# Kernel optimization log

Measured on AMD Instinct MI355X. Metric: run time of the kernel, lower is better.

Reference implementation:

```python
import jax, jax.numpy as jnp
import numpy as np

D_MODEL = 2048
SEQ_LEN = 16   # R is built for context_window=16 in the original module
BATCH = 256


def make_rotary_matrix(m, d):
    # Faithful to get_rotary_matrix: theta = 10000 ** (-2*(i-1)/d)  (note the i-1 bug kept)
    pos = np.arange(m, dtype=np.float64)[:, None]            # [m,1]
    i = np.arange(d // 2, dtype=np.float64)[None, :]         # [1,d/2]
    theta = 10000.0 ** (-2.0 * (i - 1.0) / d)
    ang = pos * theta                                         # [m, d/2]
    cos, sin = np.cos(ang), np.sin(ang)
    R = np.zeros((m, d, d), dtype=np.float32)
    idx = np.arange(d // 2)
    R[:, 2 * idx, 2 * idx] = cos
    R[:, 2 * idx, 2 * idx + 1] = -sin
    R[:, 2 * idx + 1, 2 * idx] = sin
    R[:, 2 * idx + 1, 2 * idx + 1] = cos
    return jnp.asarray(R)


def setup_inputs() -> dict:
    key = jax.random.key(0)
    kx, kq, kk, kv = jax.random.split(key, 4)
    s = 1.0 / np.sqrt(D_MODEL)
    return {
        "x": jax.random.normal(kx, (BATCH, SEQ_LEN, D_MODEL), dtype=jnp.float32),
        "w_q": jax.random.normal(kq, (D_MODEL, D_MODEL), dtype=jnp.float32) * s,
        "w_k": jax.random.normal(kk, (D_MODEL, D_MODEL), dtype=jnp.float32) * s,
        "w_v": jax.random.normal(kv, (D_MODEL, D_MODEL), dtype=jnp.float32) * s,
    }


def reference(x, w_q, w_k, w_v):
    b, m, d = x.shape
    R = make_rotary_matrix(SEQ_LEN, d)[:m]                    # [m,d,d]
    # nn.Linear(bias=False): y = x @ W^T
    q = jnp.einsum("bmd,ed->bme", x, w_q)
    k = jnp.einsum("bmd,ed->bme", x, w_k)
    v = jnp.einsum("bmd,ed->bme", x, w_v)
    # dense per-position rotary rotation via bmm: (q.transpose(0,1) @ R[:m]).transpose(0,1)
    q_rot = jnp.einsum("bmd,mde->bme", q, R)
    k_rot = jnp.einsum("bmd,mde->bme", k, R)
    # scaled_dot_product_attention (dropout treated as eval-mode / disabled)
    scores = jnp.einsum("bme,bne->bmn", q_rot, k_rot) / jnp.sqrt(jnp.float32(d))
    attn = jax.nn.softmax(scores, axis=-1)
    return jnp.einsum("bmn,bne->bme", attn, v)
```

## Files before the change

### kernel.cpp

```cpp
#include <hip/hip_runtime.h>


#define D 2048
#define SEQLEN 16
#define NBATCH 256
#define NROWS (NBATCH * SEQLEN)
#define NX (NROWS * D)
#define NW (D * D)

#define BM 128
#define BN 192
#define BK 64
#define NKT (D / BK)
#define LDSPB ((BM + BN) * BK)

typedef __attribute__((ext_vector_type(8))) short bf16x8;
typedef __attribute__((ext_vector_type(4))) float f32x4;

__device__ __forceinline__ unsigned short f32_to_bf16(float f) {
  unsigned u = __float_as_uint(f);
  unsigned r = 0x7fffu + ((u >> 16) & 1u);
  return (unsigned short)((u + r) >> 16);
}
__device__ __forceinline__ float bf16lo_to_f32(unsigned u) { return __uint_as_float(u << 16); }
__device__ __forceinline__ float bf16hi_to_f32(unsigned u) { return __uint_as_float(u & 0xffff0000u); }

__device__ __forceinline__ bool detect_f32(const ushort* __restrict__ w) {
  int crazy = 0;
#pragma unroll
  for (int i = 0; i < 64; ++i) {
    float v = __uint_as_float((unsigned)w[i] << 16);
    if (!(__builtin_fabsf(v) < 256.0f)) ++crazy;
  }
  return crazy >= 3;
}

__device__ __forceinline__ void glds16(const void* g, void* l) {
  __builtin_amdgcn_global_load_lds(
      (const __attribute__((address_space(1))) void*)g,
      (__attribute__((address_space(3))) void*)l, 16, 0, 0);
}

__global__ __launch_bounds__(256) void convert_inputs(
    const void* __restrict__ x, const void* __restrict__ wq,
    const void* __restrict__ wk, const void* __restrict__ wv,
    ushort* __restrict__ xb, ushort* __restrict__ wqb,
    ushort* __restrict__ wkb, ushort* __restrict__ wvb) {
  if (!detect_f32((const ushort*)wq)) return;
  const float* srcs[4] = {(const float*)x, (const float*)wq, (const float*)wk, (const float*)wv};
  ushort* dsts[4] = {xb, wqb, wkb, wvb};
  const int ns[4] = {NX, NW, NW, NW};
  const int stride = gridDim.x * blockDim.x;
#pragma unroll
  for (int s = 0; s < 4; ++s) {
    const float* __restrict__ src = srcs[s];
    ushort* __restrict__ dst = dsts[s];
    const int n8 = ns[s] / 8;
    for (int i = blockIdx.x * blockDim.x + threadIdx.x; i < n8; i += stride) {
      float4 a = ((const float4*)src)[i * 2];
      float4 b = ((const float4*)src)[i * 2 + 1];
      uint4 o;
      o.x = (unsigned)f32_to_bf16(a.x) | ((unsigned)f32_to_bf16(a.y) << 16);
      o.y = (unsigned)f32_to_bf16(a.z) | ((unsigned)f32_to_bf16(a.w) << 16);
      o.z = (unsigned)f32_to_bf16(b.x) | ((unsigned)f32_to_bf16(b.y) << 16);
      o.w = (unsigned)f32_to_bf16(b.z) | ((unsigned)f32_to_bf16(b.w) << 16);
      ((uint4*)dst)[i] = o;
    }
  }
}

__global__ __launch_bounds__(256, 2) void qkv_rope_gemm(
    const void* __restrict__ Xr, const void* __restrict__ Wqr,
    const void* __restrict__ Wkr, const void* __restrict__ Wvr,
    const ushort* __restrict__ xb, const ushort* __restrict__ wqb,
    const ushort* __restrict__ wkb, const ushort* __restrict__ wvb,
    ushort* __restrict__ Ov, float* __restrict__ Sp) {
  __shared__ __align__(16) ushort lds[2][LDSPB];

  const bool f32in = detect_f32((const ushort*)Wqr);
  const ushort* __restrict__ X  = f32in ? xb  : (const ushort*)Xr;
  const ushort* __restrict__ Wq = f32in ? wqb : (const ushort*)Wqr;
  const ushort* __restrict__ Wk = f32in ? wkb : (const ushort*)Wkr;
  const ushort* __restrict__ Wv = f32in ? wvb : (const ushort*)Wvr;

  const int m0 = (blockIdx.x >> 5) * BM;
  const int eb = blockIdx.x & 31;
  const int e0 = eb * 64;

  const int t = threadIdx.x;
  const int wave = t >> 6, lane = t & 63;
  const int quad = lane >> 4, l16 = lane & 15;
  const int wr = wave >> 1, wc = wave & 1;

  const int srow = t >> 3;
  const int scol = ((t & 7) ^ (srow & 7)) * 8;
  const ushort* gA = X + (size_t)(m0 + srow) * D + scol;
  const ushort* gB[6];
#pragma unroll
  for (int c = 0; c < 6; ++c) {
    const ushort* Wz = (c < 2) ? Wq : (c < 4) ? Wk : Wv;
    gB[c] = Wz + (size_t)(e0 + (c & 1) * 32 + srow) * D + scol;
  }

  f32x4 acc[4][6] = {};

  auto STAGE = [&](int b, int kt) {
    const int kc = kt * BK;
#pragma unroll
    for (int c = 0; c < 4; ++c)
      glds16(gA + (size_t)c * 32 * D + kc, &lds[b][c * 2048 + t * 8]);
#pragma unroll
    for (int c = 0; c < 6; ++c)
      glds16(gB[c] + kc, &lds[b][BM * BK + c * 2048 + t * 8]);
  };

  STAGE(0, 0);
  STAGE(1, 1);

  const int swz = (l16 & 7) << 3;

  for (int kt = 0; kt < NKT; ++kt) {
    const int cur = kt & 1;

    if (kt < NKT - 1) asm volatile("s_waitcnt vmcnt(10)" ::: "memory");
    else              asm volatile("s_waitcnt vmcnt(0)"  ::: "memory");
    __builtin_amdgcn_s_barrier();
    __builtin_amdgcn_sched_barrier(0);

    const ushort* Ab = &lds[cur][0];
    const ushort* Bb = &lds[cur][BM * BK];

    bf16x8 af2[2][4], bfr2[2][6];
#pragma unroll
    for (int ks = 0; ks < 2; ++ks) {
      const int ko = (ks * 32 + quad * 8) ^ swz;
#pragma unroll
      for (int f = 0; f < 4; ++f)
        af2[ks][f] = *(const bf16x8*)(Ab + (wr * 64 + f * 16 + l16) * 64 + ko);
#pragma unroll
      for (int g = 0; g < 6; ++g)
        bfr2[ks][g] = *(const bf16x8*)(Bb + (wc * 96 + g * 16 + l16) * 64 + ko);
    }
    asm volatile("s_waitcnt lgkmcnt(0)" ::: "memory");
    __builtin_amdgcn_s_barrier();
    if (kt + 2 < NKT) STAGE(cur, kt + 2);
    __builtin_amdgcn_sched_barrier(0);

    __builtin_amdgcn_s_setprio(1);
#pragma unroll
    for (int ks = 0; ks < 2; ++ks)
#pragma unroll
      for (int f = 0; f < 4; ++f)
#pragma unroll
        for (int g = 0; g < 6; ++g)
          acc[f][g] = __builtin_amdgcn_mfma_f32_16x16x32_bf16(
              af2[ks][f], bfr2[ks][g], acc[f][g], 0, 0, 0);
    __builtin_amdgcn_s_setprio(0);
  }

  ushort* qk_lds = &lds[0][0];
#pragma unroll
  for (int g = 0; g < 6; ++g) {
    const int ncol = wc * 96 + g * 16;
    const int z = ncol >> 6;
    const int el = (ncol & 63) + l16;
    const int eg = e0 + el;
    if (z < 2) {
      const float theta = exp2f(-0.012976281620653759f * ((float)(eg >> 1) - 1.0f));
      float cs[4], sn[4];
#pragma unroll
      for (int r = 0; r < 4; ++r)
        __sincosf((float)(quad * 4 + r) * theta, &sn[r], &cs[r]);
#pragma unroll
      for (int f = 0; f < 4; ++f) {
#pragma unroll
        for (int r = 0; r < 4; ++r) {
          float v = acc[f][g][r];
          float p = __shfl_xor(v, 1);
          float o = (eg & 1) ? (v * cs[r] - p * sn[r])
                             : (v * cs[r] + p * sn[r]);
          const int row = wr * 64 + f * 16 + quad * 4 + r;
          const int colw = el ^ ((row & 7) << 3);
          qk_lds[z * 8192 + row * 64 + colw] = f32_to_bf16(o);
        }
      }
    } else {
#pragma unroll
      for (int f = 0; f < 4; ++f) {
        const size_t rbase = (size_t)(m0 + wr * 64 + f * 16 + quad * 4) * D;
#pragma unroll
        for (int r = 0; r < 4; ++r)
          Ov[rbase + (size_t)r * D + eg] = f32_to_bf16(acc[f][g][r]);
      }
    }
  }
  __syncthreads();

  const int gb0 = (m0 >> 4);
#pragma unroll
  for (int bb = 0; bb < 2; ++bb) {
    const int bi = wave * 2 + bb;
    const int row = bi * 16 + l16;
    f32x4 s = {0.f, 0.f, 0.f, 0.f};
#pragma unroll
    for (int ks = 0; ks < 2; ++ks) {
      const int ko = (ks * 32 + quad * 8) ^ swz;
      bf16x8 aq = *(const bf16x8*)(qk_lds + row * 64 + ko);
      bf16x8 bk = *(const bf16x8*)(qk_lds + 8192 + row * 64 + ko);
      s = __builtin_amdgcn_mfma_f32_16x16x32_bf16(aq, bk, s, 0, 0, 0);
    }
    float* sp = Sp + ((size_t)(eb * NBATCH + gb0 + bi) << 8);
#pragma unroll
    for (int r = 0; r < 4; ++r)
      sp[(quad * 4 + r) * 16 + l16] = s[r];
  }
}

__global__ __launch_bounds__(256) void rope_attention(
    const float* __restrict__ Sp, const ushort* __restrict__ V,
    const void* __restrict__ Wqr, void* __restrict__ OutRaw) {
  __shared__ float at[16][16];
  const bool f32out = detect_f32((const ushort*)Wqr);
  const int b = blockIdx.x;
  const int t = threadIdx.x;

  {
    const int m = t >> 4, n = t & 15;
    float s = 0.f;
#pragma unroll
    for (int ebi = 0; ebi < 32; ++ebi)
      s += Sp[((size_t)(ebi * NBATCH + b) << 8) + t];
    s *= 0.02209708691207961f;
    float mx = s;
#pragma unroll
    for (int off = 8; off; off >>= 1) mx = fmaxf(mx, __shfl_xor(mx, off, 16));
    float e = __expf(s - mx);
    float sum = e;
#pragma unroll
    for (int off = 8; off; off >>= 1) sum += __shfl_xor(sum, off, 16);
    at[m][n] = e / sum;
  }
  __syncthreads();

  const ushort* Vb = V + (size_t)b * (SEQLEN * D);
  const int e0 = t * 8;
  uint4 vr[16];
#pragma unroll
  for (int n = 0; n < 16; ++n)
    vr[n] = *(const uint4*)(Vb + n * D + e0);

  for (int m = 0; m < 16; ++m) {
    float av[8] = {0.f, 0.f, 0.f, 0.f, 0.f, 0.f, 0.f, 0.f};
#pragma unroll
    for (int n = 0; n < 16; ++n) {
      const float a = at[m][n];
      const uint4 u = vr[n];
      av[0] = fmaf(a, bf16lo_to_f32(u.x), av[0]);
      av[1] = fmaf(a, bf16hi_to_f32(u.x), av[1]);
      av[2] = fmaf(a, bf16lo_to_f32(u.y), av[2]);
      av[3] = fmaf(a, bf16hi_to_f32(u.y), av[3]);
      av[4] = fmaf(a, bf16lo_to_f32(u.z), av[4]);
      av[5] = fmaf(a, bf16hi_to_f32(u.z), av[5]);
      av[6] = fmaf(a, bf16lo_to_f32(u.w), av[6]);
      av[7] = fmaf(a, bf16hi_to_f32(u.w), av[7]);
    }
    if (f32out) {
      float* Ob = (float*)OutRaw + (size_t)b * (SEQLEN * D) + m * D + e0;
      float4 o0 = {av[0], av[1], av[2], av[3]};
      float4 o1 = {av[4], av[5], av[6], av[7]};
      ((float4*)Ob)[0] = o0;
      ((float4*)Ob)[1] = o1;
    } else {
      uint4 o;
      o.x = (unsigned)f32_to_bf16(av[0]) | ((unsigned)f32_to_bf16(av[1]) << 16);
      o.y = (unsigned)f32_to_bf16(av[2]) | ((unsigned)f32_to_bf16(av[3]) << 16);
      o.z = (unsigned)f32_to_bf16(av[4]) | ((unsigned)f32_to_bf16(av[5]) << 16);
      o.w = (unsigned)f32_to_bf16(av[6]) | ((unsigned)f32_to_bf16(av[7]) << 16);
      *(uint4*)((ushort*)OutRaw + (size_t)b * (SEQLEN * D) + m * D + e0) = o;
    }
  }
}

extern "C" void kernel_launch(void* const* d_in, const int* in_sizes, int n_in,
                              void* d_out, int out_size, void* d_ws, size_t ws_size,
                              hipStream_t stream) {
  const void* x  = d_in[0];
  const void* wq = d_in[1];
  const void* wk = d_in[2];
  const void* wv = d_in[3];
  ushort* ws = (ushort*)d_ws;
  ushort* xb  = ws;
  ushort* wqb = ws + NX;
  ushort* wkb = ws + NX + NW;
  ushort* wvb = ws + NX + 2 * (size_t)NW;
  ushort* v   = ws + NX + 3 * (size_t)NW;
  float*  Sp  = (float*)(ws + 2 * (size_t)NX + 3 * (size_t)NW);

  convert_inputs<<<1536, 256, 0, stream>>>(x, wq, wk, wv, xb, wqb, wkb, wvb);
  qkv_rope_gemm<<<dim3(1024), 256, 0, stream>>>(x, wq, wk, wv, xb, wqb, wkb, wvb, v, Sp);
  rope_attention<<<NBATCH, 256, 0, stream>>>(Sp, v, wq, (ushort*)d_out);
}
```

Baseline: 228.9 us.

## Enlarge QKV GEMM tile to 256 rows with 512 threads and split MFMA phases

The fused QKV+RoPE GEMM block grows from 128x192 to 256x192 using 8 waves. Each block now loads one 64-row slice of each of Wq, Wk and Wv, and covers twice as many X rows, so weight tiles are shared across more rows and fewer blocks reload them. The inner loop is also restructured: B fragments are loaded once, A fragments are loaded in two halves, and each half is followed by its MFMAs between barriers, so LDS reads interleave with compute. The cost is a larger LDS footprint, about 115KB per block. That likely allows only one block per CU despite the launch bound of two, and the added barriers per k-step may cost synchronisation time.

```diff
diff --git a/kernel.cpp b/kernel.cpp
--- a/kernel.cpp
+++ b/kernel.cpp
@@ -8,7 +8,7 @@
 #define NX (NROWS * D)
 #define NW (D * D)
 
-#define BM 128
+#define BM 256
 #define BN 192
 #define BK 64
 #define NKT (D / BK)
@@ -69,13 +69,13 @@
   }
 }
 
-__global__ __launch_bounds__(256, 2) void qkv_rope_gemm(
+__global__ __launch_bounds__(512, 2) void qkv_rope_gemm(
     const void* __restrict__ Xr, const void* __restrict__ Wqr,
     const void* __restrict__ Wkr, const void* __restrict__ Wvr,
     const ushort* __restrict__ xb, const ushort* __restrict__ wqb,
     const ushort* __restrict__ wkb, const ushort* __restrict__ wvb,
     ushort* __restrict__ Ov, float* __restrict__ Sp) {
-  __shared__ __align__(16) ushort lds[2][LDSPB];
+  __shared__ __align__(16) ushort ldsraw[2 * LDSPB];
 
   const bool f32in = detect_f32((const ushort*)Wqr);
   const ushort* __restrict__ X  = f32in ? xb  : (const ushort*)Xr;
@@ -90,28 +90,27 @@
   const int t = threadIdx.x;
   const int wave = t >> 6, lane = t & 63;
   const int quad = lane >> 4, l16 = lane & 15;
-  const int wr = wave >> 1, wc = wave & 1;
+  const int wr = wave >> 2, wc = wave & 3;
 
   const int srow = t >> 3;
   const int scol = ((t & 7) ^ (srow & 7)) * 8;
   const ushort* gA = X + (size_t)(m0 + srow) * D + scol;
-  const ushort* gB[6];
-#pragma unroll
-  for (int c = 0; c < 6; ++c) {
-    const ushort* Wz = (c < 2) ? Wq : (c < 4) ? Wk : Wv;
-    gB[c] = Wz + (size_t)(e0 + (c & 1) * 32 + srow) * D + scol;
-  }
-
-  f32x4 acc[4][6] = {};
+  const ushort* gB[3];
+  gB[0] = Wq + (size_t)(e0 + srow) * D + scol;
+  gB[1] = Wk + (size_t)(e0 + srow) * D + scol;
+  gB[2] = Wv + (size_t)(e0 + srow) * D + scol;
+
+  f32x4 acc[8][3] = {};
 
   auto STAGE = [&](int b, int kt) {
+    ushort* base = ldsraw + b * LDSPB;
     const int kc = kt * BK;
 #pragma unroll
     for (int c = 0; c < 4; ++c)
-      glds16(gA + (size_t)c * 32 * D + kc, &lds[b][c * 2048 + t * 8]);
-#pragma unroll
-    for (int c = 0; c < 6; ++c)
-      glds16(gB[c] + kc, &lds[b][BM * BK + c * 2048 + t * 8]);
+      glds16(gA + (size_t)c * 64 * D + kc, base + c * 4096 + t * 8);
+#pragma unroll
+    for (int c = 0; c < 3; ++c)
+      glds16(gB[c] + kc, base + BM * BK + c * 4096 + t * 8);
   };
 
   STAGE(0, 0);
@@ -122,46 +121,51 @@
   for (int kt = 0; kt < NKT; ++kt) {
     const int cur = kt & 1;
 
-    if (kt < NKT - 1) asm volatile("s_waitcnt vmcnt(10)" ::: "memory");
-    else              asm volatile("s_waitcnt vmcnt(0)"  ::: "memory");
+    if (kt < NKT - 1) asm volatile("s_waitcnt vmcnt(7)" ::: "memory");
+    else              asm volatile("s_waitcnt vmcnt(0)" ::: "memory");
     __builtin_amdgcn_s_barrier();
     __builtin_amdgcn_sched_barrier(0);
 
-    const ushort* Ab = &lds[cur][0];
-    const ushort* Bb = &lds[cur][BM * BK];
-
-    bf16x8 af2[2][4], bfr2[2][6];
+    const ushort* Ab = ldsraw + cur * LDSPB;
+    const ushort* Bb = Ab + BM * BK;
+
 #pragma unroll
     for (int ks = 0; ks < 2; ++ks) {
       const int ko = (ks * 32 + quad * 8) ^ swz;
-#pragma unroll
-      for (int f = 0; f < 4; ++f)
-        af2[ks][f] = *(const bf16x8*)(Ab + (wr * 64 + f * 16 + l16) * 64 + ko);
-#pragma unroll
-      for (int g = 0; g < 6; ++g)
-        bfr2[ks][g] = *(const bf16x8*)(Bb + (wc * 96 + g * 16 + l16) * 64 + ko);
-    }
-    asm volatile("s_waitcnt lgkmcnt(0)" ::: "memory");
-    __builtin_amdgcn_s_barrier();
+      bf16x8 bfr[3];
+#pragma unroll
+      for (int mh = 0; mh < 2; ++mh) {
+        bf16x8 af[4];
+        if (mh == 0) {
+#pragma unroll
+          for (int g = 0; g < 3; ++g)
+            bfr[g] = *(const bf16x8*)(Bb + (wc * 48 + g * 16 + l16) * 64 + ko);
+        }
+#pragma unroll
+        for (int f = 0; f < 4; ++f)
+          af[f] = *(const bf16x8*)(Ab + (wr * 128 + (mh * 4 + f) * 16 + l16) * 64 + ko);
+        __builtin_amdgcn_sched_barrier(0);
+        __builtin_amdgcn_s_barrier();
+        asm volatile("s_waitcnt lgkmcnt(0)" ::: "memory");
+        __builtin_amdgcn_s_setprio(1);
+#pragma unroll
+        for (int f = 0; f < 4; ++f)
+#pragma unroll
+          for (int g = 0; g < 3; ++g)
+            acc[mh * 4 + f][g] = __builtin_amdgcn_mfma_f32_16x16x32_bf16(
+                af[f], bfr[g], acc[mh * 4 + f][g], 0, 0, 0);
+        __builtin_amdgcn_s_setprio(0);
+        __builtin_amdgcn_s_barrier();
+      }
+    }
+
     if (kt + 2 < NKT) STAGE(cur, kt + 2);
-    __builtin_amdgcn_sched_barrier(0);
-
-    __builtin_amdgcn_s_setprio(1);
-#pragma unroll
-    for (int ks = 0; ks < 2; ++ks)
-#pragma unroll
-      for (int f = 0; f < 4; ++f)
-#pragma unroll
-        for (int g = 0; g < 6; ++g)
-          acc[f][g] = __builtin_amdgcn_mfma_f32_16x16x32_bf16(
-              af2[ks][f], bfr2[ks][g], acc[f][g], 0, 0, 0);
-    __builtin_amdgcn_s_setprio(0);
-  }
-
-  ushort* qk_lds = &lds[0][0];
-#pragma unroll
-  for (int g = 0; g < 6; ++g) {
-    const int ncol = wc * 96 + g * 16;
+  }
+
+  ushort* qk_lds = ldsraw;
+#pragma unroll
+  for (int g = 0; g < 3; ++g) {
+    const int ncol = wc * 48 + g * 16;
     const int z = ncol >> 6;
     const int el = (ncol & 63) + l16;
     const int eg = e0 + el;
@@ -172,22 +176,22 @@
       for (int r = 0; r < 4; ++r)
         __sincosf((float)(quad * 4 + r) * theta, &sn[r], &cs[r]);
 #pragma unroll
-      for (int f = 0; f < 4; ++f) {
+      for (int f = 0; f < 8; ++f) {
 #pragma unroll
         for (int r = 0; r < 4; ++r) {
           float v = acc[f][g][r];
           float p = __shfl_xor(v, 1);
           float o = (eg & 1) ? (v * cs[r] - p * sn[r])
                              : (v * cs[r] + p * sn[r]);
-          const int row = wr * 64 + f * 16 + quad * 4 + r;
+          const int row = wr * 128 + f * 16 + quad * 4 + r;
           const int colw = el ^ ((row & 7) << 3);
-          qk_lds[z * 8192 + row * 64 + colw] = f32_to_bf16(o);
+          qk_lds[z * 16384 + row * 64 + colw] = f32_to_bf16(o);
         }
       }
     } else {
 #pragma unroll
-      for (int f = 0; f < 4; ++f) {
-        const size_t rbase = (size_t)(m0 + wr * 64 + f * 16 + quad * 4) * D;
+      for (int f = 0; f < 8; ++f) {
+        const size_t rbase = (size_t)(m0 + wr * 128 + f * 16 + quad * 4) * D;
 #pragma unroll
         for (int r = 0; r < 4; ++r)
           Ov[rbase + (size_t)r * D + eg] = f32_to_bf16(acc[f][g][r]);
@@ -206,7 +210,7 @@
     for (int ks = 0; ks < 2; ++ks) {
       const int ko = (ks * 32 + quad * 8) ^ swz;
       bf16x8 aq = *(const bf16x8*)(qk_lds + row * 64 + ko);
-      bf16x8 bk = *(const bf16x8*)(qk_lds + 8192 + row * 64 + ko);
+      bf16x8 bk = *(const bf16x8*)(qk_lds + 16384 + row * 64 + ko);
       s = __builtin_amdgcn_mfma_f32_16x16x32_bf16(aq, bk, s, 0, 0, 0);
     }
     float* sp = Sp + ((size_t)(eb * NBATCH + gb0 + bi) << 8);
@@ -297,6 +301,6 @@
   float*  Sp  = (float*)(ws + 2 * (size_t)NX + 3 * (size_t)NW);
 
   convert_inputs<<<1536, 256, 0, stream>>>(x, wq, wk, wv, xb, wqb, wkb, wvb);
-  qkv_rope_gemm<<<dim3(1024), 256, 0, stream>>>(x, wq, wk, wv, xb, wqb, wkb, wvb, v, Sp);
+  qkv_rope_gemm<<<dim3(512), 512, 0, stream>>>(x, wq, wk, wv, xb, wqb, wkb, wvb, v, Sp);
   rope_attention<<<NBATCH, 256, 0, stream>>>(Sp, v, wq, (ushort*)d_out);
 }
```

Result: slower. 242.8 us (+6.1%).
